# Performance work log

Hardware: AMD Instinct MI355X
Metric: run time of the kernel (lower is better)

The kernel has to match this reference:

```python
import jax, jax.numpy as jnp
import numpy as np

N = 2048


def setup_inputs() -> dict:
    key = jax.random.key(0)
    k1, k2 = jax.random.split(key)
    graph1 = jax.random.uniform(k1, (N, N), dtype=jnp.float32)
    graph2 = jax.random.uniform(k2, (N, N), dtype=jnp.float32)
    return {"graph1": graph1, "graph2": graph2}


def _degree_dist(adj):
    return adj.sum(axis=-1)


def _clustering(adj):
    # diag(A @ A @ A) computed without materializing the full cube:
    # tri_i = sum_j (A@A)_{ij} * A_{ji}
    a2 = adj @ adj                      # [n, n]
    tri = (a2 * adj.T).sum(axis=-1)     # [n]
    deg = adj.sum(axis=-1)
    deg = jnp.where(deg < 2, 1.0, deg)  # torch: deg[deg < 2] = 1
    return tri / (deg * (deg - 1.0))


def reference(graph1, graph2):
    d1 = _degree_dist(graph1)
    d2 = _degree_dist(graph2)
    degree_sim = jnp.exp(-jnp.abs(d1 - d2).mean())
    c1 = _clustering(graph1)
    c2 = _clustering(graph2)
    cluster_sim = jnp.exp(-jnp.abs(c1 - c2).mean())
    overall = (degree_sim + cluster_sim) / 2.0
    return (degree_sim, cluster_sim, overall)
```

## Files before the change

### kernel.cpp

```cpp
#include <hip/hip_runtime.h>

#define NN 2048

typedef unsigned short u16;
typedef unsigned char u8;
typedef __attribute__((ext_vector_type(4))) float floatx4;

__device__ __forceinline__ float fp8_to_f32(unsigned v) {
  const unsigned e = (v >> 3) & 15, m = v & 7;
  const float norm = __uint_as_float(((e + 120u) << 23) | (m << 20));
  const float sub = (float)m * 0.001953125f;
  return e == 0 ? sub : norm;
}

__device__ __forceinline__ void load_lds16(const u8* g, u8* l) {
  __builtin_amdgcn_global_load_lds(
      (const __attribute__((address_space(1))) unsigned int*)g,
      (__attribute__((address_space(3))) unsigned int*)l,
      16, 0, 0);
}

__global__ __launch_bounds__(256) void prep_kernel(
    const float* __restrict__ A1, const float* __restrict__ A2,
    u8* __restrict__ A8, u8* __restrict__ A8T,
    float* __restrict__ degp, float* __restrict__ tri) {
  __shared__ unsigned Tl[64 * 17];
  const int bx = blockIdx.x, by = blockIdx.y, bz = blockIdx.z;
  const float* __restrict__ A = bz ? A2 : A1;
  u8* __restrict__ ab = A8 + (size_t)bz * (NN * (size_t)NN);
  u8* __restrict__ at = A8T + (size_t)bz * (NN * (size_t)NN);
  float* __restrict__ dp = degp + (size_t)bz * (32 * NN);
  const int t = threadIdx.x;
  const int r0 = by * 64, c0 = bx * 64;
  const int q = t >> 4, cs = t & 15;

  if (bx == 0 && t < 64) tri[bz * NN + by * 64 + t] = 0.f;

  unsigned rowpack[4];
#pragma unroll
  for (int d = 0; d < 4; ++d) {
    const int r = 4 * q + d;
    const float4 fv = *(const float4*)(A + (size_t)(r0 + r) * NN + c0 + cs * 4);
    int pk = __builtin_amdgcn_cvt_pk_fp8_f32(fv.x, fv.y, 0, false);
    pk = __builtin_amdgcn_cvt_pk_fp8_f32(fv.z, fv.w, pk, true);
    rowpack[d] = (unsigned)pk;
    *(unsigned*)(ab + (size_t)(r0 + r) * NN + c0 + cs * 4) = (unsigned)pk;
    float s = fv.x + fv.y + fv.z + fv.w;
    s += __shfl_xor(s, 1); s += __shfl_xor(s, 2);
    s += __shfl_xor(s, 4); s += __shfl_xor(s, 8);
    if (cs == 0) dp[(size_t)(r0 + r) * 32 + bx] = s;
  }
#pragma unroll
  for (int e = 0; e < 4; ++e) {
    const unsigned tc = ((rowpack[0] >> (8 * e)) & 0xFFu) |
                        (((rowpack[1] >> (8 * e)) & 0xFFu) << 8) |
                        (((rowpack[2] >> (8 * e)) & 0xFFu) << 16) |
                        (((rowpack[3] >> (8 * e)) & 0xFFu) << 24);
    Tl[(4 * cs + e) * 17 + q] = tc;
  }
  __syncthreads();
#pragma unroll
  for (int p = 0; p < 2; ++p) {
    const int rp = p * 32 + (t >> 3);
    const int mm = t & 7;
    uint2 v;
    v.x = Tl[rp * 17 + 2 * mm];
    v.y = Tl[rp * 17 + 2 * mm + 1];
    *(uint2*)(at + (size_t)(c0 + rp) * NN + r0 + mm * 8) = v;
  }
}

#define MFMA_BODY(PB)                                                      \
  {                                                                        \
    long aL[4][2], bL[4][2];                                               \
    _Pragma("unroll")                                                      \
    for (int tm = 0; tm < 4; ++tm) {                                       \
      aL[tm][0] = *(const long*)(smem + (PB) + aoff[tm][0]);               \
      aL[tm][1] = *(const long*)(smem + (PB) + aoff[tm][1]);               \
    }                                                                      \
    _Pragma("unroll")                                                      \
    for (int tn = 0; tn < 4; ++tn) {                                       \
      bL[tn][0] = *(const long*)(smem + (PB) + boff[tn][0]);               \
      bL[tn][1] = *(const long*)(smem + (PB) + boff[tn][1]);               \
    }                                                                      \
    _Pragma("unroll")                                                      \
    for (int tm = 0; tm < 4; ++tm)                                         \
      _Pragma("unroll")                                                    \
      for (int tn = 0; tn < 4; ++tn) {                                     \
        acc[tm][tn] = __builtin_amdgcn_mfma_f32_16x16x32_fp8_fp8(          \
            aL[tm][0], bL[tn][0], acc[tm][tn], 0, 0, 0);                   \
        acc[tm][tn] = __builtin_amdgcn_mfma_f32_16x16x32_fp8_fp8(          \
            aL[tm][1], bL[tn][1], acc[tm][tn], 0, 0, 0);                   \
      }                                                                    \
  }

#define PREFETCH(KK, DB)                                                   \
  load_lds16(gA0 + (KK), smem + (DB) + sA0);                               \
  load_lds16(gA1 + (KK), smem + (DB) + sA1);                               \
  load_lds16(gB0 + (KK), smem + (DB) + sB0);                               \
  load_lds16(gB1 + (KK), smem + (DB) + sB1);

#define FENCE asm volatile("" ::: "memory")

__global__ __launch_bounds__(256, 4) void gemm_tri_kernel(
    const u8* __restrict__ A8, const u8* __restrict__ A8T,
    float* __restrict__ tri) {
  __shared__ __align__(16) u8 smem[32768];

  const int tid = threadIdx.x;
  const int w = tid >> 6, lane = tid & 63;
  const int wm = w >> 1, wn = w & 1;
  const int cl = lane & 15, g = lane >> 4;
  const int i0 = blockIdx.y * 128, j0 = blockIdx.x * 128;
  const int mz = blockIdx.z >> 1, kz = blockIdx.z & 1;
  const size_t mat = (size_t)mz * (NN * (size_t)NN);
  const u8* __restrict__ Am = A8 + mat;
  const u8* __restrict__ ATm = A8T + mat;
  float* __restrict__ triM = tri + mz * NN;

  const int s0 = (w * 2 + 0) * 64 + lane;
  const int s1 = (w * 2 + 1) * 64 + lane;
  const int r0s = s0 >> 2, c0s = (s0 & 3) ^ ((r0s >> 1) & 3);
  const int r1s = s1 >> 2, c1s = (s1 & 3) ^ ((r1s >> 1) & 3);
  const int kbase = kz * 1024;
  const u8* gA0 = Am + (size_t)(i0 + r0s) * NN + kbase + c0s * 16;
  const u8* gA1 = Am + (size_t)(i0 + r1s) * NN + kbase + c1s * 16;
  const u8* gB0 = ATm + (size_t)(j0 + r0s) * NN + kbase + c0s * 16;
  const u8* gB1 = ATm + (size_t)(j0 + r1s) * NN + kbase + c1s * 16;
  const int sA0 = (w * 2 + 0) * 1024, sA1 = (w * 2 + 1) * 1024;
  const int sB0 = 8192 + sA0, sB1 = 8192 + sA1;

  const int rsw = (cl >> 1) & 3;
  const int sub = (g & 1) * 8, ch = g >> 1;
  int aoff[4][2], boff[4][2];
#pragma unroll
  for (int tm = 0; tm < 4; ++tm) {
    const int r = wm * 64 + tm * 16 + cl;
#pragma unroll
    for (int h = 0; h < 2; ++h)
      aoff[tm][h] = r * 64 + (((2 * h + ch) ^ rsw) * 16) + sub;
  }
#pragma unroll
  for (int tn = 0; tn < 4; ++tn) {
    const int r = wn * 64 + tn * 16 + cl;
#pragma unroll
    for (int h = 0; h < 2; ++h)
      boff[tn][h] = 8192 + r * 64 + (((2 * h + ch) ^ rsw) * 16) + sub;
  }

  floatx4 acc[4][4] = {};

  PREFETCH(0, 0)

#pragma unroll 1
  for (int d = 0; d < 7; ++d) {
    FENCE; __builtin_amdgcn_s_barrier(); FENCE;
    PREFETCH((2 * d + 1) * 64, 16384)
    __builtin_amdgcn_s_waitcnt(0x0F74);
    FENCE; __builtin_amdgcn_s_barrier(); FENCE;
    MFMA_BODY(0)
    FENCE; __builtin_amdgcn_s_barrier(); FENCE;
    PREFETCH((2 * d + 2) * 64, 0)
    __builtin_amdgcn_s_waitcnt(0x0F74);
    FENCE; __builtin_amdgcn_s_barrier(); FENCE;
    MFMA_BODY(16384)
  }
  FENCE; __builtin_amdgcn_s_barrier(); FENCE;
  PREFETCH(15 * 64, 16384)
  __builtin_amdgcn_s_waitcnt(0x0F74);
  FENCE; __builtin_amdgcn_s_barrier(); FENCE;
  MFMA_BODY(0)
  FENCE; __builtin_amdgcn_s_barrier(); FENCE;
  __builtin_amdgcn_s_waitcnt(0x0F70);
  FENCE; __builtin_amdgcn_s_barrier(); FENCE;
  MFMA_BODY(16384)

  __syncthreads();
#pragma unroll
  for (int it = 0; it < 4; ++it) {
    const int idx = tid + it * 256;
    const int r = idx >> 3, co = (idx & 7) * 16;
    *(uint4*)(smem + r * 144 + co) =
        *(const uint4*)(ATm + (size_t)(i0 + r) * NN + j0 + co);
  }
  __syncthreads();

#pragma unroll
  for (int tm = 0; tm < 4; ++tm) {
#pragma unroll
    for (int reg = 0; reg < 4; ++reg) {
      const int rloc = wm * 64 + tm * 16 + g * 4 + reg;
      float v = 0.f;
#pragma unroll
      for (int tn = 0; tn < 4; ++tn) {
        const int cloc = wn * 64 + tn * 16 + cl;
        v += acc[tm][tn][reg] * fp8_to_f32(smem[rloc * 144 + cloc]);
      }
      v += __shfl_xor(v, 1);
      v += __shfl_xor(v, 2);
      v += __shfl_xor(v, 4);
      v += __shfl_xor(v, 8);
      if (cl == 0) atomicAdd(&triM[i0 + rloc], v);
    }
  }
}

__global__ __launch_bounds__(1024) void finalize1_kernel(
    const float* __restrict__ degp, const float* __restrict__ tri,
    float* __restrict__ part) {
  __shared__ float red[32];
  const int t = threadIdx.x;
  const int r = blockIdx.x * 128 + (t >> 3);
  const int q = (t & 7) * 4;
  const float4 v1 = *(const float4*)(degp + (size_t)r * 32 + q);
  const float4 v2 = *(const float4*)(degp + 32 * NN + (size_t)r * 32 + q);
  float d1 = v1.x + v1.y + v1.z + v1.w;
  float d2 = v2.x + v2.y + v2.z + v2.w;
#pragma unroll
  for (int m = 1; m < 8; m <<= 1) {
    d1 += __shfl_xor(d1, m);
    d2 += __shfl_xor(d2, m);
  }
  float sdd = 0.f, scc = 0.f;
  if ((t & 7) == 0) {
    const float t1 = tri[r], t2 = tri[NN + r];
    const float e1 = d1 < 2.f ? 1.f : d1;
    const float e2 = d2 < 2.f ? 1.f : d2;
    sdd = fabsf(d1 - d2);
    scc = fabsf(t1 / (e1 * (e1 - 1.f)) - t2 / (e2 * (e2 - 1.f)));
  }
#pragma unroll
  for (int m = 8; m < 64; m <<= 1) {
    sdd += __shfl_xor(sdd, m);
    scc += __shfl_xor(scc, m);
  }
  const int wv = t >> 6, ln = t & 63;
  if (ln == 0) { red[wv] = sdd; red[16 + wv] = scc; }
  __syncthreads();
  if (t == 0) {
    float a = 0.f, b = 0.f;
#pragma unroll
    for (int i = 0; i < 16; ++i) { a += red[i]; b += red[16 + i]; }
    part[blockIdx.x * 2 + 0] = a;
    part[blockIdx.x * 2 + 1] = b;
  }
}

__global__ void finalize2_kernel(const float* __restrict__ part,
                                 float* __restrict__ out) {
  if (threadIdx.x == 0) {
    float a = 0.f, b = 0.f;
#pragma unroll
    for (int i = 0; i < 16; ++i) { a += part[i * 2]; b += part[i * 2 + 1]; }
    const float ds = expf(-a * (1.f / (float)NN));
    const float cs = expf(-b * (1.f / (float)NN));
    out[0] = ds;
    out[1] = cs;
    out[2] = 0.5f * (ds + cs);
  }
}

extern "C" void kernel_launch(void* const* d_in, const int* in_sizes, int n_in,
                              void* d_out, int out_size, void* d_ws, size_t ws_size,
                              hipStream_t stream) {
  (void)in_sizes; (void)n_in; (void)out_size; (void)ws_size;
  const float* A1 = (const float*)d_in[0];
  const float* A2 = (const float*)d_in[1];
  float* out = (float*)d_out;

  u8* A8 = (u8*)d_ws;
  u8* A8T = A8 + 2 * (size_t)NN * NN;
  float* tri = (float*)(A8T + 2 * (size_t)NN * NN);
  float* degp = tri + 2 * NN;
  float* part = degp + 2 * 32 * NN;

  prep_kernel<<<dim3(32, 32, 2), 256, 0, stream>>>(A1, A2, A8, A8T, degp, tri);
  gemm_tri_kernel<<<dim3(16, 16, 4), 256, 0, stream>>>(A8, A8T, tri);
  finalize1_kernel<<<16, 1024, 0, stream>>>(degp, tri, part);
  finalize2_kernel<<<1, 64, 0, stream>>>(part, out);
}
```

Measured before the change: 115.7 us.

## Switch GEMM inner loop to 32x32x64 scaled fp8 MFMA tiles

Replaces the 16x16x32 fp8 MFMA tiling (4x4 tiles, two k-steps each) with 2x2 tiles of the gfx950 32x32x64 f8f6f4 scaled MFMA using unit scales. LDS fragments are now loaded as 16-byte reads instead of 8-byte reads, and the epilogue row mapping and shuffle reduction are adapted to the 32-lane layout. The goal is higher MFMA throughput per instruction and fewer LDS load instructions. In exchange, occupancy is lowered to 3 waves per SIMD in launch bounds, and the new swizzle mapping may change LDS bank conflicts.

```diff
diff --git a/kernel.cpp b/kernel.cpp
--- a/kernel.cpp
+++ b/kernel.cpp
@@ -4,7 +4,8 @@
 
 typedef unsigned short u16;
 typedef unsigned char u8;
-typedef __attribute__((ext_vector_type(4))) float floatx4;
+typedef __attribute__((ext_vector_type(8))) int intx8;
+typedef __attribute__((ext_vector_type(16))) float floatx16;
 
 __device__ __forceinline__ float fp8_to_f32(unsigned v) {
   const unsigned e = (v >> 3) & 15, m = v & 7;
@@ -70,28 +71,25 @@
   }
 }
 
-#define MFMA_BODY(PB)                                                      \
-  {                                                                        \
-    long aL[4][2], bL[4][2];                                               \
-    _Pragma("unroll")                                                      \
-    for (int tm = 0; tm < 4; ++tm) {                                       \
-      aL[tm][0] = *(const long*)(smem + (PB) + aoff[tm][0]);               \
-      aL[tm][1] = *(const long*)(smem + (PB) + aoff[tm][1]);               \
-    }                                                                      \
-    _Pragma("unroll")                                                      \
-    for (int tn = 0; tn < 4; ++tn) {                                       \
-      bL[tn][0] = *(const long*)(smem + (PB) + boff[tn][0]);               \
-      bL[tn][1] = *(const long*)(smem + (PB) + boff[tn][1]);               \
-    }                                                                      \
-    _Pragma("unroll")                                                      \
-    for (int tm = 0; tm < 4; ++tm)                                         \
-      _Pragma("unroll")                                                    \
-      for (int tn = 0; tn < 4; ++tn) {                                     \
-        acc[tm][tn] = __builtin_amdgcn_mfma_f32_16x16x32_fp8_fp8(          \
-            aL[tm][0], bL[tn][0], acc[tm][tn], 0, 0, 0);                   \
-        acc[tm][tn] = __builtin_amdgcn_mfma_f32_16x16x32_fp8_fp8(          \
-            aL[tm][1], bL[tn][1], acc[tm][tn], 0, 0, 0);                   \
-      }                                                                    \
+#define MFMA_BODY(PB)                                                         \
+  {                                                                           \
+    intx8 aF[2], bF[2];                                                       \
+    _Pragma("unroll")                                                         \
+    for (int tm = 0; tm < 2; ++tm) {                                          \
+      *(uint4*)&aF[tm] = *(const uint4*)(smem + (PB) + aoff[tm][0]);          \
+      *((uint4*)&aF[tm] + 1) = *(const uint4*)(smem + (PB) + aoff[tm][1]);    \
+    }                                                                         \
+    _Pragma("unroll")                                                         \
+    for (int tn = 0; tn < 2; ++tn) {                                          \
+      *(uint4*)&bF[tn] = *(const uint4*)(smem + (PB) + boff[tn][0]);          \
+      *((uint4*)&bF[tn] + 1) = *(const uint4*)(smem + (PB) + boff[tn][1]);    \
+    }                                                                         \
+    _Pragma("unroll")                                                         \
+    for (int tm = 0; tm < 2; ++tm)                                            \
+      _Pragma("unroll")                                                       \
+      for (int tn = 0; tn < 2; ++tn)                                          \
+        acc[tm][tn] = __builtin_amdgcn_mfma_scale_f32_32x32x64_f8f6f4(        \
+            aF[tm], bF[tn], acc[tm][tn], 0, 0, 0, 0x7F7F7F7F, 0, 0x7F7F7F7F); \
   }
 
 #define PREFETCH(KK, DB)                                                   \
@@ -102,7 +100,7 @@
 
 #define FENCE asm volatile("" ::: "memory")
 
-__global__ __launch_bounds__(256, 4) void gemm_tri_kernel(
+__global__ __launch_bounds__(256, 3) void gemm_tri_kernel(
     const u8* __restrict__ A8, const u8* __restrict__ A8T,
     float* __restrict__ tri) {
   __shared__ __align__(16) u8 smem[32768];
@@ -110,7 +108,7 @@
   const int tid = threadIdx.x;
   const int w = tid >> 6, lane = tid & 63;
   const int wm = w >> 1, wn = w & 1;
-  const int cl = lane & 15, g = lane >> 4;
+  const int l31 = lane & 31, kg = lane >> 5;
   const int i0 = blockIdx.y * 128, j0 = blockIdx.x * 128;
   const int mz = blockIdx.z >> 1, kz = blockIdx.z & 1;
   const size_t mat = (size_t)mz * (NN * (size_t)NN);
@@ -130,25 +128,24 @@
   const int sA0 = (w * 2 + 0) * 1024, sA1 = (w * 2 + 1) * 1024;
   const int sB0 = 8192 + sA0, sB1 = 8192 + sA1;
 
-  const int rsw = (cl >> 1) & 3;
-  const int sub = (g & 1) * 8, ch = g >> 1;
-  int aoff[4][2], boff[4][2];
-#pragma unroll
-  for (int tm = 0; tm < 4; ++tm) {
-    const int r = wm * 64 + tm * 16 + cl;
+  const int rsw = (l31 >> 1) & 3;
+  int aoff[2][2], boff[2][2];
+#pragma unroll
+  for (int tm = 0; tm < 2; ++tm) {
+    const int r = wm * 64 + tm * 32 + l31;
 #pragma unroll
     for (int h = 0; h < 2; ++h)
-      aoff[tm][h] = r * 64 + (((2 * h + ch) ^ rsw) * 16) + sub;
-  }
-#pragma unroll
-  for (int tn = 0; tn < 4; ++tn) {
-    const int r = wn * 64 + tn * 16 + cl;
+      aoff[tm][h] = r * 64 + (((2 * kg + h) ^ rsw) * 16);
+  }
+#pragma unroll
+  for (int tn = 0; tn < 2; ++tn) {
+    const int r = wn * 64 + tn * 32 + l31;
 #pragma unroll
     for (int h = 0; h < 2; ++h)
-      boff[tn][h] = 8192 + r * 64 + (((2 * h + ch) ^ rsw) * 16) + sub;
-  }
-
-  floatx4 acc[4][4] = {};
+      boff[tn][h] = 8192 + r * 64 + (((2 * kg + h) ^ rsw) * 16);
+  }
+
+  floatx16 acc[2][2] = {};
 
   PREFETCH(0, 0)
 
@@ -186,21 +183,22 @@
   __syncthreads();
 
 #pragma unroll
-  for (int tm = 0; tm < 4; ++tm) {
-#pragma unroll
-    for (int reg = 0; reg < 4; ++reg) {
-      const int rloc = wm * 64 + tm * 16 + g * 4 + reg;
+  for (int tm = 0; tm < 2; ++tm) {
+#pragma unroll
+    for (int reg = 0; reg < 16; ++reg) {
+      const int rloc = wm * 64 + tm * 32 + (reg & 3) + 8 * (reg >> 2) + 4 * kg;
       float v = 0.f;
 #pragma unroll
-      for (int tn = 0; tn < 4; ++tn) {
-        const int cloc = wn * 64 + tn * 16 + cl;
+      for (int tn = 0; tn < 2; ++tn) {
+        const int cloc = wn * 64 + tn * 32 + l31;
         v += acc[tm][tn][reg] * fp8_to_f32(smem[rloc * 144 + cloc]);
       }
       v += __shfl_xor(v, 1);
       v += __shfl_xor(v, 2);
       v += __shfl_xor(v, 4);
       v += __shfl_xor(v, 8);
-      if (cl == 0) atomicAdd(&triM[i0 + rloc], v);
+      v += __shfl_xor(v, 16);
+      if (l31 == 0) atomicAdd(&triM[i0 + rloc], v);
     }
   }
 }
```

Measured after the change: 131.8 us. 13.9% more time.

## Triple-buffer the LDS k-pipeline with one barrier per stage in gemm_tri

Applied to the files above, without the earlier changes.

Moves the fp8 GEMM main loop from double to triple buffering in LDS, growing shared memory from 32 KB to 48 KB. Each k-step now issues its async prefetch two stages ahead and uses a single wait plus barrier instead of two barriers. The goal is to hide more global-load latency and cut synchronisation stalls. The larger LDS footprint may lower the number of resident blocks per CU. The epilogue also reads A^T bytes through a dword LDS load and shift instead of a byte load.

```diff
diff --git a/kernel.cpp b/kernel.cpp
--- a/kernel.cpp
+++ b/kernel.cpp
@@ -101,11 +101,14 @@
   load_lds16(gB1 + (KK), smem + (DB) + sB1);
 
 #define FENCE asm volatile("" ::: "memory")
+#define WAIT4 __builtin_amdgcn_s_waitcnt(0x0F74)
+#define WAIT0 __builtin_amdgcn_s_waitcnt(0x0F70)
+#define BAR do { FENCE; __builtin_amdgcn_s_barrier(); FENCE; } while (0)
 
 __global__ __launch_bounds__(256, 4) void gemm_tri_kernel(
     const u8* __restrict__ A8, const u8* __restrict__ A8T,
     float* __restrict__ tri) {
-  __shared__ __align__(16) u8 smem[32768];
+  __shared__ __align__(16) u8 smem[49152];
 
   const int tid = threadIdx.x;
   const int w = tid >> 6, lane = tid & 63;
@@ -151,29 +154,31 @@
   floatx4 acc[4][4] = {};
 
   PREFETCH(0, 0)
+  PREFETCH(64, 16384)
 
 #pragma unroll 1
-  for (int d = 0; d < 7; ++d) {
-    FENCE; __builtin_amdgcn_s_barrier(); FENCE;
-    PREFETCH((2 * d + 1) * 64, 16384)
-    __builtin_amdgcn_s_waitcnt(0x0F74);
-    FENCE; __builtin_amdgcn_s_barrier(); FENCE;
+  for (int d = 0; d < 4; ++d) {
+    const int kk = d * 192;
+    WAIT4; BAR;
+    PREFETCH(kk + 128, 32768)
     MFMA_BODY(0)
-    FENCE; __builtin_amdgcn_s_barrier(); FENCE;
-    PREFETCH((2 * d + 2) * 64, 0)
-    __builtin_amdgcn_s_waitcnt(0x0F74);
-    FENCE; __builtin_amdgcn_s_barrier(); FENCE;
+    WAIT4; BAR;
+    PREFETCH(kk + 192, 0)
     MFMA_BODY(16384)
-  }
-  FENCE; __builtin_amdgcn_s_barrier(); FENCE;
-  PREFETCH(15 * 64, 16384)
-  __builtin_amdgcn_s_waitcnt(0x0F74);
-  FENCE; __builtin_amdgcn_s_barrier(); FENCE;
+    WAIT4; BAR;
+    PREFETCH(kk + 256, 16384)
+    MFMA_BODY(32768)
+  }
+  WAIT4; BAR;
+  PREFETCH(14 * 64, 32768)
   MFMA_BODY(0)
-  FENCE; __builtin_amdgcn_s_barrier(); FENCE;
-  __builtin_amdgcn_s_waitcnt(0x0F70);
-  FENCE; __builtin_amdgcn_s_barrier(); FENCE;
+  WAIT4; BAR;
+  PREFETCH(15 * 64, 0)
   MFMA_BODY(16384)
+  WAIT4; BAR;
+  MFMA_BODY(32768)
+  WAIT0; BAR;
+  MFMA_BODY(0)
 
   __syncthreads();
 #pragma unroll
@@ -194,7 +199,9 @@
 #pragma unroll
       for (int tn = 0; tn < 4; ++tn) {
         const int cloc = wn * 64 + tn * 16 + cl;
-        v += acc[tm][tn][reg] * fp8_to_f32(smem[rloc * 144 + cloc]);
+        const unsigned dw =
+            *(const unsigned*)(smem + rloc * 144 + (cloc & ~3));
+        v += acc[tm][tn][reg] * fp8_to_f32((dw >> ((cloc & 3) * 8)) & 0xFFu);
       }
       v += __shfl_xor(v, 1);
       v += __shfl_xor(v, 2);
```

After: 118.2 us. +2.1%, slower.

## Load GEMM fragments directly from global into double-buffered registers instead of LDS

Applied to the files above, without the earlier changes.

The GEMM main loop drops the LDS staging (global_load_lds, swizzled LDS layout and barriers). Each wave now loads its own 16-byte A and B fragments straight from global memory into a two-slot register buffer, overlapping the next step's loads with the current step's MFMAs. This removes barrier and LDS traffic, and cuts LDS to 18 KB, used only by the epilogue. In exchange, waves sharing rows fetch the same data redundantly through the cache, register pressure rises (occupancy hint drops to 3), and the runtime-indexed register slots (s&1 in a non-unrolled loop) risk scratch spills. The epilogue also reads the transposed tile as dwords and extracts bytes.

```diff
diff --git a/kernel.cpp b/kernel.cpp
--- a/kernel.cpp
+++ b/kernel.cpp
@@ -11,13 +11,6 @@
   const float norm = __uint_as_float(((e + 120u) << 23) | (m << 20));
   const float sub = (float)m * 0.001953125f;
   return e == 0 ? sub : norm;
-}
-
-__device__ __forceinline__ void load_lds16(const u8* g, u8* l) {
-  __builtin_amdgcn_global_load_lds(
-      (const __attribute__((address_space(1))) unsigned int*)g,
-      (__attribute__((address_space(3))) unsigned int*)l,
-      16, 0, 0);
 }
 
 __global__ __launch_bounds__(256) void prep_kernel(
@@ -70,42 +63,32 @@
   }
 }
 
-#define MFMA_BODY(PB)                                                      \
-  {                                                                        \
-    long aL[4][2], bL[4][2];                                               \
-    _Pragma("unroll")                                                      \
-    for (int tm = 0; tm < 4; ++tm) {                                       \
-      aL[tm][0] = *(const long*)(smem + (PB) + aoff[tm][0]);               \
-      aL[tm][1] = *(const long*)(smem + (PB) + aoff[tm][1]);               \
-    }                                                                      \
+#define LOADSTEP(SL, OFF)                                                  \
+  _Pragma("unroll")                                                        \
+  for (int tm = 0; tm < 4; ++tm)                                           \
+    aR[SL][tm] = *(const uint4*)(pA[tm] + (OFF));                          \
+  _Pragma("unroll")                                                        \
+  for (int tn = 0; tn < 4; ++tn)                                           \
+    bR[SL][tn] = *(const uint4*)(pB[tn] + (OFF));
+
+#define MFMAS(SL)                                                          \
+  _Pragma("unroll")                                                        \
+  for (int tm = 0; tm < 4; ++tm) {                                         \
+    const long* ap = (const long*)&aR[SL][tm];                             \
     _Pragma("unroll")                                                      \
     for (int tn = 0; tn < 4; ++tn) {                                       \
-      bL[tn][0] = *(const long*)(smem + (PB) + boff[tn][0]);               \
-      bL[tn][1] = *(const long*)(smem + (PB) + boff[tn][1]);               \
+      const long* bp = (const long*)&bR[SL][tn];                           \
+      acc[tm][tn] = __builtin_amdgcn_mfma_f32_16x16x32_fp8_fp8(            \
+          ap[0], bp[0], acc[tm][tn], 0, 0, 0);                             \
+      acc[tm][tn] = __builtin_amdgcn_mfma_f32_16x16x32_fp8_fp8(            \
+          ap[1], bp[1], acc[tm][tn], 0, 0, 0);                             \
     }                                                                      \
-    _Pragma("unroll")                                                      \
-    for (int tm = 0; tm < 4; ++tm)                                         \
-      _Pragma("unroll")                                                    \
-      for (int tn = 0; tn < 4; ++tn) {                                     \
-        acc[tm][tn] = __builtin_amdgcn_mfma_f32_16x16x32_fp8_fp8(          \
-            aL[tm][0], bL[tn][0], acc[tm][tn], 0, 0, 0);                   \
-        acc[tm][tn] = __builtin_amdgcn_mfma_f32_16x16x32_fp8_fp8(          \
-            aL[tm][1], bL[tn][1], acc[tm][tn], 0, 0, 0);                   \
-      }                                                                    \
-  }
-
-#define PREFETCH(KK, DB)                                                   \
-  load_lds16(gA0 + (KK), smem + (DB) + sA0);                               \
-  load_lds16(gA1 + (KK), smem + (DB) + sA1);                               \
-  load_lds16(gB0 + (KK), smem + (DB) + sB0);                               \
-  load_lds16(gB1 + (KK), smem + (DB) + sB1);
-
-#define FENCE asm volatile("" ::: "memory")
-
-__global__ __launch_bounds__(256, 4) void gemm_tri_kernel(
+  }
+
+__global__ __launch_bounds__(256, 3) void gemm_tri_kernel(
     const u8* __restrict__ A8, const u8* __restrict__ A8T,
     float* __restrict__ tri) {
-  __shared__ __align__(16) u8 smem[32768];
+  __shared__ __align__(16) u8 smem[18432];
 
   const int tid = threadIdx.x;
   const int w = tid >> 6, lane = tid & 63;
@@ -117,63 +100,30 @@
   const u8* __restrict__ Am = A8 + mat;
   const u8* __restrict__ ATm = A8T + mat;
   float* __restrict__ triM = tri + mz * NN;
-
-  const int s0 = (w * 2 + 0) * 64 + lane;
-  const int s1 = (w * 2 + 1) * 64 + lane;
-  const int r0s = s0 >> 2, c0s = (s0 & 3) ^ ((r0s >> 1) & 3);
-  const int r1s = s1 >> 2, c1s = (s1 & 3) ^ ((r1s >> 1) & 3);
   const int kbase = kz * 1024;
-  const u8* gA0 = Am + (size_t)(i0 + r0s) * NN + kbase + c0s * 16;
-  const u8* gA1 = Am + (size_t)(i0 + r1s) * NN + kbase + c1s * 16;
-  const u8* gB0 = ATm + (size_t)(j0 + r0s) * NN + kbase + c0s * 16;
-  const u8* gB1 = ATm + (size_t)(j0 + r1s) * NN + kbase + c1s * 16;
-  const int sA0 = (w * 2 + 0) * 1024, sA1 = (w * 2 + 1) * 1024;
-  const int sB0 = 8192 + sA0, sB1 = 8192 + sA1;
-
-  const int rsw = (cl >> 1) & 3;
-  const int sub = (g & 1) * 8, ch = g >> 1;
-  int aoff[4][2], boff[4][2];
-#pragma unroll
-  for (int tm = 0; tm < 4; ++tm) {
-    const int r = wm * 64 + tm * 16 + cl;
-#pragma unroll
-    for (int h = 0; h < 2; ++h)
-      aoff[tm][h] = r * 64 + (((2 * h + ch) ^ rsw) * 16) + sub;
-  }
-#pragma unroll
-  for (int tn = 0; tn < 4; ++tn) {
-    const int r = wn * 64 + tn * 16 + cl;
-#pragma unroll
-    for (int h = 0; h < 2; ++h)
-      boff[tn][h] = 8192 + r * 64 + (((2 * h + ch) ^ rsw) * 16) + sub;
-  }
+
+  const u8* pA[4];
+  const u8* pB[4];
+#pragma unroll
+  for (int tm = 0; tm < 4; ++tm)
+    pA[tm] = Am + (size_t)(i0 + wm * 64 + tm * 16 + cl) * NN + kbase + g * 16;
+#pragma unroll
+  for (int tn = 0; tn < 4; ++tn)
+    pB[tn] = ATm + (size_t)(j0 + wn * 64 + tn * 16 + cl) * NN + kbase + g * 16;
 
   floatx4 acc[4][4] = {};
-
-  PREFETCH(0, 0)
+  uint4 aR[2][4], bR[2][4];
+
+  LOADSTEP(0, 0)
 
 #pragma unroll 1
-  for (int d = 0; d < 7; ++d) {
-    FENCE; __builtin_amdgcn_s_barrier(); FENCE;
-    PREFETCH((2 * d + 1) * 64, 16384)
-    __builtin_amdgcn_s_waitcnt(0x0F74);
-    FENCE; __builtin_amdgcn_s_barrier(); FENCE;
-    MFMA_BODY(0)
-    FENCE; __builtin_amdgcn_s_barrier(); FENCE;
-    PREFETCH((2 * d + 2) * 64, 0)
-    __builtin_amdgcn_s_waitcnt(0x0F74);
-    FENCE; __builtin_amdgcn_s_barrier(); FENCE;
-    MFMA_BODY(16384)
-  }
-  FENCE; __builtin_amdgcn_s_barrier(); FENCE;
-  PREFETCH(15 * 64, 16384)
-  __builtin_amdgcn_s_waitcnt(0x0F74);
-  FENCE; __builtin_amdgcn_s_barrier(); FENCE;
-  MFMA_BODY(0)
-  FENCE; __builtin_amdgcn_s_barrier(); FENCE;
-  __builtin_amdgcn_s_waitcnt(0x0F70);
-  FENCE; __builtin_amdgcn_s_barrier(); FENCE;
-  MFMA_BODY(16384)
+  for (int s = 0; s < 15; ++s) {
+    const int cur = s & 1, nxt = cur ^ 1;
+    const int off = (s + 1) * 64;
+    LOADSTEP(nxt, off)
+    MFMAS(cur)
+  }
+  MFMAS(1)
 
   __syncthreads();
 #pragma unroll
@@ -194,7 +144,9 @@
 #pragma unroll
       for (int tn = 0; tn < 4; ++tn) {
         const int cloc = wn * 64 + tn * 16 + cl;
-        v += acc[tm][tn][reg] * fp8_to_f32(smem[rloc * 144 + cloc]);
+        const unsigned dw =
+            *(const unsigned*)(smem + rloc * 144 + (cloc & ~3));
+        v += acc[tm][tn][reg] * fp8_to_f32((dw >> ((cloc & 3) * 8)) & 0xFFu);
       }
       v += __shfl_xor(v, 1);
       v += __shfl_xor(v, 2);
```

Result: slower. 270.1 us (+133.5%).
